# Kernel tuning notes

Measured on AMD Instinct MI355X. Metric: run time of the kernel, lower is better.

The kernel has to match this reference:

```python
import jax, jax.numpy as jnp
import numpy as np
import math

HIDDEN = 512
NUM_HEADS = 8
HEAD_DIM = HIDDEN // NUM_HEADS
NUM_BUCKETS = 32
MAX_DISTANCE = 128


def _relative_position_bucket(rel_pos, bidirectional=True):
    # rel_pos: int32 [S, T]
    num_buckets = NUM_BUCKETS
    ret = 0
    if bidirectional:
        num_buckets //= 2
        ret = (rel_pos > 0).astype(jnp.int32) * num_buckets
        rel_pos = jnp.abs(rel_pos)
    else:
        rel_pos = -jnp.minimum(rel_pos, 0)
    max_exact = num_buckets // 2
    is_small = rel_pos < max_exact
    # guard log(0); result unused where is_small
    safe = jnp.maximum(rel_pos, 1).astype(jnp.float32)
    val_if_large = max_exact + (
        jnp.log(safe / max_exact) / math.log(MAX_DISTANCE / max_exact) * (num_buckets - max_exact)
    ).astype(jnp.int32)
    val_if_large = jnp.minimum(val_if_large, num_buckets - 1)
    return ret + jnp.where(is_small, rel_pos, val_if_large)


def setup_inputs() -> dict:
    key = jax.random.key(0)
    ks = jax.random.split(key, 6)
    B, S = 4, 2048
    std = 1.0 / math.sqrt(HIDDEN)
    inp = {
        "x": jax.random.normal(ks[0], (B, S, HIDDEN), dtype=jnp.float32),
        "Wq": jax.random.normal(ks[1], (HIDDEN, HIDDEN), dtype=jnp.float32) * std,
        "Wk": jax.random.normal(ks[2], (HIDDEN, HIDDEN), dtype=jnp.float32) * std,
        "Wv": jax.random.normal(ks[3], (HIDDEN, HIDDEN), dtype=jnp.float32) * std,
        "Wo": jax.random.normal(ks[4], (HIDDEN, HIDDEN), dtype=jnp.float32) * std,
        "bias_table": jax.random.normal(ks[5], (NUM_BUCKETS, NUM_HEADS), dtype=jnp.float32) * 0.02,
    }
    return inp


def reference(x, Wq, Wk, Wv, Wo, bias_table):
    # x: [B, S, HIDDEN]; weights: [HIDDEN, HIDDEN] (out = x @ W.T semantics folded as x @ W here
    # -- weights are random so orientation is a convention; we use x @ W).
    B, S, _ = x.shape
    T = S  # self-attention, context=None
    scale = HEAD_DIM ** -0.5

    def split_heads(t, L):
        return t.reshape(B, L, NUM_HEADS, HEAD_DIM).transpose(0, 2, 1, 3)  # [B,H,L,D]

    q = split_heads(x @ Wq, S)
    k = split_heads(x @ Wk, T)
    v = split_heads(x @ Wv, T)

    # relative position bias: [1, H, S, T]
    rel = jnp.arange(T, dtype=jnp.int32)[None, :] - jnp.arange(S, dtype=jnp.int32)[:, None]
    buckets = _relative_position_bucket(rel, bidirectional=True)  # [S, T]
    pos_bias = bias_table[buckets]  # [S, T, H]
    pos_bias = pos_bias.transpose(2, 0, 1)[None]  # [1, H, S, T]

    attn = jnp.einsum("bhsd,bhtd->bhst", q, k) * scale + pos_bias
    attn = jax.nn.softmax(attn, axis=-1)  # dropout = identity (eval)
    out = jnp.einsum("bhst,bhtd->bhsd", attn, v)
    out = out.transpose(0, 2, 1, 3).reshape(B, S, HIDDEN)
    return out @ Wo
```

## Files before the change

kernel.cpp:

```cpp
#include <hip/hip_runtime.h>
#include <hip/hip_bf16.h>
#include <math.h>

#define HIDDEN 512
#define NHEADS 8
#define HDIM 64
#define SLEN 2048
#define BATCH 4
#define NROWS (BATCH*SLEN)
#define RTAB (2*SLEN-1)
#define LOG2E 1.44269504088896340736f
#define SCALE_L2E (0.125f * LOG2E)

typedef _Float16 f16;
typedef f16 f16x8 __attribute__((ext_vector_type(8)));
typedef float f32x4 __attribute__((ext_vector_type(4)));
typedef unsigned short u16;
typedef unsigned int u32;
typedef u16 u16x4 __attribute__((ext_vector_type(4)));
typedef u16 u16x8 __attribute__((ext_vector_type(8)));
typedef u32 u32x4 __attribute__((ext_vector_type(4)));

__global__ __launch_bounds__(256) void bias_precompute(
    const float* __restrict__ bias_table, float* __restrict__ biasrel) {
  int i = blockIdx.x * 256 + threadIdx.x;
  if (i >= NHEADS * RTAB) return;
  int h = i / RTAB;
  int idx = i - h * RTAB;
  int rel = idx - (SLEN - 1);
  int ret = rel > 0 ? 16 : 0;
  int a = rel < 0 ? -rel : rel;
  int bidx;
  if (a < 8) {
    bidx = a;
  } else {
    float val = logf((float)a * 0.125f) / logf(16.0f) * 8.0f;
    bidx = 8 + (int)val;
    if (bidx > 15) bidx = 15;
  }
  biasrel[i] = bias_table[(ret + bidx) * NHEADS + h] * LOG2E;
}

__global__ __launch_bounds__(256) void conv_x(
    const float* __restrict__ x, u16* __restrict__ xh) {
  int i = blockIdx.x * 256 + threadIdx.x;
  const float4* p = (const float4*)(x + (size_t)i * 8);
  float4 a = p[0], b = p[1];
  u16x8 o;
  f16 t0 = (f16)a.x; o[0] = *(u16*)&t0;
  f16 t1 = (f16)a.y; o[1] = *(u16*)&t1;
  f16 t2 = (f16)a.z; o[2] = *(u16*)&t2;
  f16 t3 = (f16)a.w; o[3] = *(u16*)&t3;
  f16 t4 = (f16)b.x; o[4] = *(u16*)&t4;
  f16 t5 = (f16)b.y; o[5] = *(u16*)&t5;
  f16 t6 = (f16)b.z; o[6] = *(u16*)&t6;
  f16 t7 = (f16)b.w; o[7] = *(u16*)&t7;
  *(u16x8*)(xh + (size_t)i * 8) = o;
}

__global__ __launch_bounds__(256) void conv_w(
    const float* __restrict__ Wq, const float* __restrict__ Wk,
    const float* __restrict__ Wv, const float* __restrict__ Wo,
    u16* __restrict__ Wt) {
  const float* W = blockIdx.y == 0 ? Wq : blockIdx.y == 1 ? Wk
                 : blockIdx.y == 2 ? Wv : Wo;
  u16* dst = Wt + (size_t)blockIdx.y * HIDDEN * HIDDEN;
  int t = blockIdx.x * 256 + threadIdx.x;
  int k = t >> 6, n0 = (t & 63) << 3;
  const float4* p = (const float4*)(W + (size_t)k * HIDDEN + n0);
  float4 a = p[0], b = p[1];
  float vals[8] = {a.x, a.y, a.z, a.w, b.x, b.y, b.z, b.w};
#pragma unroll
  for (int j = 0; j < 8; ++j) {
    f16 hv = (f16)vals[j];
    dst[(size_t)(n0 + j) * HIDDEN + k] = *(u16*)&hv;
  }
}

__global__ __launch_bounds__(256) void gemm_mfma(
    const u16* __restrict__ A, const u16* __restrict__ Wt0,
    const u16* __restrict__ Wt1, const u16* __restrict__ Wt2,
    void* __restrict__ O, int mode) {
  __shared__ u16 sm[2 * 128 * 72];
  u16 (*As)[72] = (u16(*)[72])sm;
  u16 (*Bs)[72] = (u16(*)[72])(sm + 128 * 72);
  const u16* Wt = blockIdx.z == 0 ? Wt0 : blockIdx.z == 1 ? Wt1 : Wt2;
  const int tid = threadIdx.x;
  const int w = tid >> 6, l = tid & 63;
  const int lr = l & 15, lg = l >> 4;
  const int wr = w >> 1, wc = w & 1;
  const int m0 = blockIdx.x << 7, n0 = blockIdx.y << 7;
  const int vtmode = (mode == 1) && (blockIdx.z == 2);

  f32x4 acc[4][4] = {};

  u16x8 areg[4], breg[4];
#pragma unroll
  for (int e = 0; e < 4; ++e) {
    int c = (e << 8) + tid;
    int row = c >> 3, g = c & 7;
    areg[e] = *(const u16x8*)(A + (size_t)(m0 + row) * HIDDEN + (g << 3));
    breg[e] = *(const u16x8*)(Wt + (size_t)(n0 + row) * HIDDEN + (g << 3));
  }

  for (int k0 = 0; k0 < HIDDEN; k0 += 64) {
    __syncthreads();
#pragma unroll
    for (int e = 0; e < 4; ++e) {
      int c = (e << 8) + tid;
      int row = c >> 3, g = c & 7;
      *(u16x8*)&As[row][g << 3] = areg[e];
      *(u16x8*)&Bs[row][g << 3] = breg[e];
    }
    __syncthreads();
    if (k0 + 64 < HIDDEN) {
#pragma unroll
      for (int e = 0; e < 4; ++e) {
        int c = (e << 8) + tid;
        int row = c >> 3, g = c & 7;
        areg[e] = *(const u16x8*)(A + (size_t)(m0 + row) * HIDDEN + k0 + 64 + (g << 3));
        breg[e] = *(const u16x8*)(Wt + (size_t)(n0 + row) * HIDDEN + k0 + 64 + (g << 3));
      }
    }
#pragma unroll
    for (int kk = 0; kk < 64; kk += 32) {
      f16x8 af[4], bf[4];
#pragma unroll
      for (int mt = 0; mt < 4; ++mt)
        af[mt] = *(const f16x8*)&As[(wr << 6) + (mt << 4) + lr][kk + (lg << 3)];
#pragma unroll
      for (int nt = 0; nt < 4; ++nt)
        bf[nt] = *(const f16x8*)&Bs[(wc << 6) + (nt << 4) + lr][kk + (lg << 3)];
      if (!vtmode) {
#pragma unroll
        for (int mt = 0; mt < 4; ++mt)
#pragma unroll
          for (int nt = 0; nt < 4; ++nt)
            acc[mt][nt] = __builtin_amdgcn_mfma_f32_16x16x32_f16(
                af[mt], bf[nt], acc[mt][nt], 0, 0, 0);
      } else {
#pragma unroll
        for (int i = 0; i < 4; ++i)
#pragma unroll
          for (int j = 0; j < 4; ++j)
            acc[i][j] = __builtin_amdgcn_mfma_f32_16x16x32_f16(
                bf[i], af[j], acc[i][j], 0, 0, 0);
      }
    }
  }

  if (mode == 0) {
    float* Of = (float*)O;
#pragma unroll
    for (int mt = 0; mt < 4; ++mt)
#pragma unroll
      for (int nt = 0; nt < 4; ++nt)
#pragma unroll
        for (int r = 0; r < 4; ++r) {
          int m = m0 + (wr << 6) + (mt << 4) + (lg << 2) + r;
          int n = n0 + (wc << 6) + (nt << 4) + lr;
          Of[(size_t)m * HIDDEN + n] = acc[mt][nt][r];
        }
  } else if (!vtmode) {
    u16* O16 = (u16*)O + (size_t)blockIdx.z * NROWS * HIDDEN;
    const float osc = (blockIdx.z == 0) ? SCALE_L2E : 1.0f;
#pragma unroll
    for (int mt = 0; mt < 4; ++mt)
#pragma unroll
      for (int nt = 0; nt < 4; ++nt)
#pragma unroll
        for (int r = 0; r < 4; ++r) {
          int m = m0 + (wr << 6) + (mt << 4) + (lg << 2) + r;
          int n = n0 + (wc << 6) + (nt << 4) + lr;
          int b = m >> 11, s = m & (SLEN - 1);
          int h = n >> 6, d = n & 63;
          f16 hv = (f16)(acc[mt][nt][r] * osc);
          O16[(((size_t)b * NHEADS + h) * SLEN + s) * HDIM + d] = *(u16*)&hv;
        }
  } else {
    __syncthreads();
    u16* tt = sm;
#pragma unroll
    for (int i = 0; i < 4; ++i)
#pragma unroll
      for (int j = 0; j < 4; ++j)
#pragma unroll
        for (int r = 0; r < 4; ++r) {
          int nl = (wc << 6) + (i << 4) + (lg << 2) + r;
          int ml = (wr << 6) + (j << 4) + lr;
          f16 hv = (f16)acc[i][j][r];
          tt[nl * 136 + ml] = *(u16*)&hv;
        }
    __syncthreads();
    u16* O16 = (u16*)O + (size_t)2 * NROWS * HIDDEN;
    int nl = tid >> 1, half = tid & 1;
    int n = n0 + nl;
    int h = n >> 6, d = n & 63;
    int b = m0 >> 11, s_base = m0 & (SLEN - 1);
    u16* orow = O16 + (((size_t)b * NHEADS + h) * HDIM + d) * SLEN + s_base;
    const u16* trow = tt + nl * 136;
#pragma unroll
    for (int c = 0; c < 8; ++c) {
      int v_off = (half << 6) + (c << 3);
      int c0 = (v_off & ~31) | (((v_off >> 3) & 3) << 2);
      u16x4 lo = *(const u16x4*)(trow + c0);
      u16x4 hi = *(const u16x4*)(trow + c0 + 16);
      u16x8 st;
#pragma unroll
      for (int j = 0; j < 4; ++j) { st[j] = lo[j]; st[j + 4] = hi[j]; }
      *(u16x8*)(orow + v_off) = st;
    }
  }
}

__global__ __launch_bounds__(256) void flash_attn_mfma(
    const u16* __restrict__ qg, const u16* __restrict__ kg,
    const u16* __restrict__ vtg, const float* __restrict__ biasrel,
    u16* __restrict__ attn_out) {
  __shared__ u16 Ks[2][64][72];
  __shared__ u16 Vt[2][64][72];

  const int tid = threadIdx.x;
  const int w = tid >> 6, l = tid & 63;
  const int lr = l & 15, lg = l >> 4;

  int bid = blockIdx.x;
  int xcd = bid & 7, idx = bid >> 3;
  int bh = (xcd << 2) + (idx >> 4);
  int bx = idx & 15;
  int h = bh & 7, b = bh >> 3;
  int q0 = bx << 7;

  const u16* qp = qg + (size_t)bh * (SLEN * HDIM);
  const u16* kp = kg + (size_t)bh * (SLEN * HDIM);
  const u16* vp = vtg + (size_t)bh * (HDIM * SLEN);

  const float bias_pos = biasrel[h * RTAB + 2 * (SLEN - 1)];
  const float bias_neg = biasrel[h * RTAB];

  f16x8 aq[2][2];
#pragma unroll
  for (int sub = 0; sub < 2; ++sub) {
    const u16* qrow = qp + (size_t)(q0 + (w << 5) + (sub << 4) + lr) * HDIM + (lg << 3);
    aq[sub][0] = *(const f16x8*)(qrow);
    aq[sub][1] = *(const f16x8*)(qrow + 32);
  }

  const float* bb = biasrel + h * RTAB + (SLEN - 1) + (lg << 2) - lr - q0 - (w << 5);

  f32x4 acc[2][4] = {};
  float l_run[2] = {0.f, 0.f};

  u16x8 kreg[2], vreg[2];
#pragma unroll
  for (int e = 0; e < 2; ++e) {
    int c = tid + (e << 8);
    int row = c >> 3, c8 = (c & 7) << 3;
    kreg[e] = *(const u16x8*)(kp + (size_t)row * HDIM + c8);
    vreg[e] = *(const u16x8*)(vp + (size_t)row * SLEN + c8);
  }
#pragma unroll
  for (int e = 0; e < 2; ++e) {
    int c = tid + (e << 8);
    int row = c >> 3, c8 = (c & 7) << 3;
    *(u16x8*)&Ks[0][row][c8] = kreg[e];
    *(u16x8*)&Vt[0][row][c8] = vreg[e];
  }
#pragma unroll
  for (int e = 0; e < 2; ++e) {
    int c = tid + (e << 8);
    int row = c >> 3, c8 = (c & 7) << 3;
    kreg[e] = *(const u16x8*)(kp + (size_t)(64 + row) * HDIM + c8);
    vreg[e] = *(const u16x8*)(vp + (size_t)row * SLEN + 64 + c8);
  }
  __syncthreads();

  int cur = 0;
  for (int t0 = 0; t0 < SLEN; t0 += 64) {
    if (t0 + 64 < SLEN) {
#pragma unroll
      for (int e = 0; e < 2; ++e) {
        int c = tid + (e << 8);
        int row = c >> 3, c8 = (c & 7) << 3;
        *(u16x8*)&Ks[cur ^ 1][row][c8] = kreg[e];
        *(u16x8*)&Vt[cur ^ 1][row][c8] = vreg[e];
      }
      if (t0 + 128 < SLEN) {
#pragma unroll
        for (int e = 0; e < 2; ++e) {
          int c = tid + (e << 8);
          int row = c >> 3, c8 = (c & 7) << 3;
          kreg[e] = *(const u16x8*)(kp + (size_t)(t0 + 128 + row) * HDIM + c8);
          vreg[e] = *(const u16x8*)(vp + (size_t)row * SLEN + t0 + 128 + c8);
        }
      }
    }

    int dtq = t0 - q0;
    f32x4 sc[2][4];
    if (dtq >= 256 || dtq <= -192) {
      float c = (dtq > 0) ? bias_pos : bias_neg;
      f32x4 cv = {c, c, c, c};
#pragma unroll
      for (int sub = 0; sub < 2; ++sub)
#pragma unroll
        for (int ct = 0; ct < 4; ++ct) sc[sub][ct] = cv;
    } else {
#pragma unroll
      for (int sub = 0; sub < 2; ++sub)
#pragma unroll
        for (int ct = 0; ct < 4; ++ct)
#pragma unroll
          for (int r = 0; r < 4; ++r)
            sc[sub][ct][r] = bb[t0 + (ct << 4) + r - (sub << 4)];
    }

    f16x8 kf[4][2];
#pragma unroll
    for (int ct = 0; ct < 4; ++ct) {
      kf[ct][0] = *(const f16x8*)&Ks[cur][(ct << 4) + lr][lg << 3];
      kf[ct][1] = *(const f16x8*)&Ks[cur][(ct << 4) + lr][32 + (lg << 3)];
    }

    __builtin_amdgcn_s_setprio(1);
#pragma unroll
    for (int sub = 0; sub < 2; ++sub)
#pragma unroll
      for (int ct = 0; ct < 4; ++ct) {
        sc[sub][ct] = __builtin_amdgcn_mfma_f32_16x16x32_f16(
            kf[ct][0], aq[sub][0], sc[sub][ct], 0, 0, 0);
        sc[sub][ct] = __builtin_amdgcn_mfma_f32_16x16x32_f16(
            kf[ct][1], aq[sub][1], sc[sub][ct], 0, 0, 0);
      }
    __builtin_amdgcn_s_setprio(0);

#pragma unroll
    for (int sub = 0; sub < 2; ++sub) {
      float rs = 0.f;
#pragma unroll
      for (int ct = 0; ct < 4; ++ct)
#pragma unroll
        for (int r = 0; r < 4; ++r) {
          float pe = __builtin_amdgcn_exp2f(sc[sub][ct][r]);
          sc[sub][ct][r] = pe;
          rs += pe;
        }
      l_run[sub] += rs;
    }

    f16x8 vf[2][4];
#pragma unroll
    for (int kb = 0; kb < 2; ++kb)
#pragma unroll
      for (int dt = 0; dt < 4; ++dt)
        vf[kb][dt] = *(const f16x8*)&Vt[cur][(dt << 4) + lr][(kb << 5) + (lg << 3)];

    __builtin_amdgcn_s_setprio(1);
#pragma unroll
    for (int sub = 0; sub < 2; ++sub)
#pragma unroll
      for (int kb = 0; kb < 2; ++kb) {
        u32 a0 = __builtin_bit_cast(u32,
            __builtin_amdgcn_cvt_pkrtz(sc[sub][2 * kb][0], sc[sub][2 * kb][1]));
        u32 a1 = __builtin_bit_cast(u32,
            __builtin_amdgcn_cvt_pkrtz(sc[sub][2 * kb][2], sc[sub][2 * kb][3]));
        u32 a2 = __builtin_bit_cast(u32,
            __builtin_amdgcn_cvt_pkrtz(sc[sub][2 * kb + 1][0], sc[sub][2 * kb + 1][1]));
        u32 a3 = __builtin_bit_cast(u32,
            __builtin_amdgcn_cvt_pkrtz(sc[sub][2 * kb + 1][2], sc[sub][2 * kb + 1][3]));
        u32x4 pk = {a0, a1, a2, a3};
        f16x8 pa = __builtin_bit_cast(f16x8, pk);
#pragma unroll
        for (int dt = 0; dt < 4; ++dt)
          acc[sub][dt] = __builtin_amdgcn_mfma_f32_16x16x32_f16(
              pa, vf[kb][dt], acc[sub][dt], 0, 0, 0);
      }
    __builtin_amdgcn_s_setprio(0);

    __syncthreads();
    cur ^= 1;
  }

#pragma unroll
  for (int sub = 0; sub < 2; ++sub) {
    float lt = l_run[sub];
    lt += __shfl_xor(lt, 16, 64);
    lt += __shfl_xor(lt, 32, 64);
    float linv[4];
#pragma unroll
    for (int r = 0; r < 4; ++r) linv[r] = 1.f / __shfl(lt, (lg << 2) + r, 16);
    u16* op = attn_out +
              ((size_t)(b * SLEN) + q0 + (w << 5) + (sub << 4)) * HIDDEN + (h << 6);
#pragma unroll
    for (int r = 0; r < 4; ++r)
#pragma unroll
      for (int dt = 0; dt < 4; ++dt) {
        f16 hv = (f16)(acc[sub][dt][r] * linv[r]);
        op[(size_t)((lg << 2) + r) * HIDDEN + (dt << 4) + lr] = *(u16*)&hv;
      }
  }
}

extern "C" void kernel_launch(void* const* d_in, const int* in_sizes, int n_in,
                              void* d_out, int out_size, void* d_ws, size_t ws_size,
                              hipStream_t stream) {
  const float* x          = (const float*)d_in[0];
  const float* Wq         = (const float*)d_in[1];
  const float* Wk         = (const float*)d_in[2];
  const float* Wv         = (const float*)d_in[3];
  const float* Wo         = (const float*)d_in[4];
  const float* bias_table = (const float*)d_in[5];
  float* out = (float*)d_out;

  u16* xh   = (u16*)d_ws;
  u16* wt   = xh + (size_t)NROWS * HIDDEN;
  u16* qkv  = wt + (size_t)4 * HIDDEN * HIDDEN;
  u16* attno_h = qkv + (size_t)3 * NROWS * HIDDEN;
  float* biasrel = (float*)(attno_h + (size_t)NROWS * HIDDEN);

  u16* qb = qkv;
  u16* kb = qkv + (size_t)NROWS * HIDDEN;
  u16* vb = qkv + (size_t)2 * NROWS * HIDDEN;

  bias_precompute<<<(NHEADS * RTAB + 255) / 256, 256, 0, stream>>>(bias_table, biasrel);
  conv_x<<<NROWS * HIDDEN / 8 / 256, 256, 0, stream>>>(x, xh);
  conv_w<<<dim3(HIDDEN * HIDDEN / 8 / 256, 4), 256, 0, stream>>>(Wq, Wk, Wv, Wo, wt);

  u16* wtq = wt;
  u16* wtk = wt + (size_t)HIDDEN * HIDDEN;
  u16* wtv = wt + (size_t)2 * HIDDEN * HIDDEN;
  u16* wto = wt + (size_t)3 * HIDDEN * HIDDEN;

  gemm_mfma<<<dim3(NROWS / 128, HIDDEN / 128, 3), 256, 0, stream>>>(
      xh, wtq, wtk, wtv, qkv, 1);

  flash_attn_mfma<<<SLEN / 128 * BATCH * NHEADS, 256, 0, stream>>>(
      qb, kb, vb, biasrel, attno_h);

  gemm_mfma<<<dim3(NROWS / 128, HIDDEN / 128, 1), 256, 0, stream>>>(
      attno_h, wto, wto, wto, out, 0);
}
```

Baseline: 105.6 us.

## Use direct global-to-LDS loads with XOR-swizzled layout in QKV projection GEMM

The QKV projection GEMM (mode 1) now loads A and W tiles straight into LDS with global_load_lds, skipping the register staging step. To keep LDS reads free of bank conflicts without padding, the fp16 conversion kernels write x and the transposed weights in an XOR-swizzled chunk order, and the MFMA fragment reads undo that swizzle. The mode-0 output GEMM keeps register staging but un-swizzles W on load. The mode-1 path drops the software prefetch overlap and uses single buffering, so load latency may be less hidden.

```diff
diff --git a/kernel.cpp b/kernel.cpp
--- a/kernel.cpp
+++ b/kernel.cpp
@@ -20,6 +20,13 @@
 typedef u16 u16x4 __attribute__((ext_vector_type(4)));
 typedef u16 u16x8 __attribute__((ext_vector_type(8)));
 typedef u32 u32x4 __attribute__((ext_vector_type(4)));
+
+typedef const __attribute__((address_space(1))) void gvoid;
+typedef __attribute__((address_space(3))) void lvoid;
+
+static __device__ __forceinline__ void gload16(const void* g, void* l) {
+  __builtin_amdgcn_global_load_lds((gvoid*)g, (lvoid*)l, 16, 0, 0);
+}
 
 __global__ __launch_bounds__(256) void bias_precompute(
     const float* __restrict__ bias_table, float* __restrict__ biasrel) {
@@ -55,7 +62,9 @@
   f16 t5 = (f16)b.y; o[5] = *(u16*)&t5;
   f16 t6 = (f16)b.z; o[6] = *(u16*)&t6;
   f16 t7 = (f16)b.w; o[7] = *(u16*)&t7;
-  *(u16x8*)(xh + (size_t)i * 8) = o;
+  int m = i >> 6;
+  int ch = (i & 63) ^ (m & 7);
+  *(u16x8*)(xh + (size_t)m * HIDDEN + (ch << 3)) = o;
 }
 
 __global__ __launch_bounds__(256) void conv_w(
@@ -72,8 +81,10 @@
   float vals[8] = {a.x, a.y, a.z, a.w, b.x, b.y, b.z, b.w};
 #pragma unroll
   for (int j = 0; j < 8; ++j) {
+    int n = n0 + j;
+    int chsw = (k >> 3) ^ (n & 7);
     f16 hv = (f16)vals[j];
-    dst[(size_t)(n0 + j) * HIDDEN + k] = *(u16*)&hv;
+    dst[(size_t)n * HIDDEN + (chsw << 3) + (k & 7)] = *(u16*)&hv;
   }
 }
 
@@ -82,8 +93,6 @@
     const u16* __restrict__ Wt1, const u16* __restrict__ Wt2,
     void* __restrict__ O, int mode) {
   __shared__ u16 sm[2 * 128 * 72];
-  u16 (*As)[72] = (u16(*)[72])sm;
-  u16 (*Bs)[72] = (u16(*)[72])(sm + 128 * 72);
   const u16* Wt = blockIdx.z == 0 ? Wt0 : blockIdx.z == 1 ? Wt1 : Wt2;
   const int tid = threadIdx.x;
   const int w = tid >> 6, l = tid & 63;
@@ -94,59 +103,101 @@
 
   f32x4 acc[4][4] = {};
 
-  u16x8 areg[4], breg[4];
-#pragma unroll
-  for (int e = 0; e < 4; ++e) {
-    int c = (e << 8) + tid;
-    int row = c >> 3, g = c & 7;
-    areg[e] = *(const u16x8*)(A + (size_t)(m0 + row) * HIDDEN + (g << 3));
-    breg[e] = *(const u16x8*)(Wt + (size_t)(n0 + row) * HIDDEN + (g << 3));
-  }
-
-  for (int k0 = 0; k0 < HIDDEN; k0 += 64) {
-    __syncthreads();
+  if (mode == 1) {
+    u16* AsL = sm;
+    u16* BsL = sm + 128 * 64;
+    const int gr = (l >> 3), gc = (l & 7) << 3;
+    for (int k0 = 0; k0 < HIDDEN; k0 += 64) {
+#pragma unroll
+      for (int i = 0; i < 4; ++i) {
+        int r0 = (w << 5) + (i << 3);
+        gload16(A + (size_t)(m0 + r0 + gr) * HIDDEN + k0 + gc, AsL + (r0 << 6));
+        gload16(Wt + (size_t)(n0 + r0 + gr) * HIDDEN + k0 + gc, BsL + (r0 << 6));
+      }
+      __syncthreads();
+#pragma unroll
+      for (int kk = 0; kk < 64; kk += 32) {
+        f16x8 af[4], bf[4];
+#pragma unroll
+        for (int mt = 0; mt < 4; ++mt) {
+          int row = (wr << 6) + (mt << 4) + lr;
+          af[mt] = *(const f16x8*)(AsL + (row << 6) +
+                                   ((((kk >> 3) + lg) ^ (lr & 7)) << 3));
+        }
+#pragma unroll
+        for (int nt = 0; nt < 4; ++nt) {
+          int row = (wc << 6) + (nt << 4) + lr;
+          bf[nt] = *(const f16x8*)(BsL + (row << 6) +
+                                   ((((kk >> 3) + lg) ^ (lr & 7)) << 3));
+        }
+        if (!vtmode) {
+#pragma unroll
+          for (int mt = 0; mt < 4; ++mt)
+#pragma unroll
+            for (int nt = 0; nt < 4; ++nt)
+              acc[mt][nt] = __builtin_amdgcn_mfma_f32_16x16x32_f16(
+                  af[mt], bf[nt], acc[mt][nt], 0, 0, 0);
+        } else {
+#pragma unroll
+          for (int i = 0; i < 4; ++i)
+#pragma unroll
+            for (int j = 0; j < 4; ++j)
+              acc[i][j] = __builtin_amdgcn_mfma_f32_16x16x32_f16(
+                  bf[i], af[j], acc[i][j], 0, 0, 0);
+        }
+      }
+      __syncthreads();
+    }
+  } else {
+    u16 (*As)[72] = (u16(*)[72])sm;
+    u16 (*Bs)[72] = (u16(*)[72])(sm + 128 * 72);
+    u16x8 areg[4], breg[4];
 #pragma unroll
     for (int e = 0; e < 4; ++e) {
       int c = (e << 8) + tid;
       int row = c >> 3, g = c & 7;
-      *(u16x8*)&As[row][g << 3] = areg[e];
-      *(u16x8*)&Bs[row][g << 3] = breg[e];
-    }
-    __syncthreads();
-    if (k0 + 64 < HIDDEN) {
+      areg[e] = *(const u16x8*)(A + (size_t)(m0 + row) * HIDDEN + (g << 3));
+      breg[e] = *(const u16x8*)(Wt + (size_t)(n0 + row) * HIDDEN +
+                                ((g ^ (row & 7)) << 3));
+    }
+    for (int k0 = 0; k0 < HIDDEN; k0 += 64) {
+      __syncthreads();
 #pragma unroll
       for (int e = 0; e < 4; ++e) {
         int c = (e << 8) + tid;
         int row = c >> 3, g = c & 7;
-        areg[e] = *(const u16x8*)(A + (size_t)(m0 + row) * HIDDEN + k0 + 64 + (g << 3));
-        breg[e] = *(const u16x8*)(Wt + (size_t)(n0 + row) * HIDDEN + k0 + 64 + (g << 3));
-      }
-    }
-#pragma unroll
-    for (int kk = 0; kk < 64; kk += 32) {
-      f16x8 af[4], bf[4];
-#pragma unroll
-      for (int mt = 0; mt < 4; ++mt)
-        af[mt] = *(const f16x8*)&As[(wr << 6) + (mt << 4) + lr][kk + (lg << 3)];
-#pragma unroll
-      for (int nt = 0; nt < 4; ++nt)
-        bf[nt] = *(const f16x8*)&Bs[(wc << 6) + (nt << 4) + lr][kk + (lg << 3)];
-      if (!vtmode) {
+        *(u16x8*)&As[row][g << 3] = areg[e];
+        *(u16x8*)&Bs[row][g << 3] = breg[e];
+      }
+      __syncthreads();
+      if (k0 + 64 < HIDDEN) {
+#pragma unroll
+        for (int e = 0; e < 4; ++e) {
+          int c = (e << 8) + tid;
+          int row = c >> 3, g = c & 7;
+          areg[e] = *(const u16x8*)(A + (size_t)(m0 + row) * HIDDEN + k0 + 64 + (g << 3));
+          breg[e] = *(const u16x8*)(Wt + (size_t)(n0 + row) * HIDDEN + k0 + 64 +
+                                    ((g ^ (row & 7)) << 3));
+        }
+      }
+#pragma unroll
+      for (int kk = 0; kk < 64; kk += 32) {
+        f16x8 af[4], bf[4];
+#pragma unroll
+        for (int mt = 0; mt < 4; ++mt)
+          af[mt] = *(const f16x8*)&As[(wr << 6) + (mt << 4) + lr][kk + (lg << 3)];
+#pragma unroll
+        for (int nt = 0; nt < 4; ++nt)
+          bf[nt] = *(const f16x8*)&Bs[(wc << 6) + (nt << 4) + lr][kk + (lg << 3)];
 #pragma unroll
         for (int mt = 0; mt < 4; ++mt)
 #pragma unroll
           for (int nt = 0; nt < 4; ++nt)
             acc[mt][nt] = __builtin_amdgcn_mfma_f32_16x16x32_f16(
                 af[mt], bf[nt], acc[mt][nt], 0, 0, 0);
-      } else {
-#pragma unroll
-        for (int i = 0; i < 4; ++i)
-#pragma unroll
-          for (int j = 0; j < 4; ++j)
-            acc[i][j] = __builtin_amdgcn_mfma_f32_16x16x32_f16(
-                bf[i], af[j], acc[i][j], 0, 0, 0);
-      }
-    }
+      }
+    }
+    __syncthreads();
   }
 
   if (mode == 0) {
@@ -178,7 +229,6 @@
           O16[(((size_t)b * NHEADS + h) * SLEN + s) * HDIM + d] = *(u16*)&hv;
         }
   } else {
-    __syncthreads();
     u16* tt = sm;
 #pragma unroll
     for (int i = 0; i < 4; ++i)
```

Result: no change. 107.6 us (+1.9%).

## Split key tiles across wave pairs and reduce partial attention outputs in LDS

Applied to the files above, without the earlier changes.

Waves are regrouped into two query groups of 64 rows each, and the two waves in a group take alternate 64-key tiles. Each wave therefore reuses every loaded K/V fragment across four query sub-tiles instead of two, cutting LDS fragment reads per MFMA. At the end the partial accumulators and row sums from the odd-key waves go through shared memory and are added into the even-key waves before normalization. This adds a final LDS reduction and barrier and raises register pressure (acc[4][4]). Half the waves also sit idle on each tile iteration, which may reduce overlap.

```diff
diff --git a/kernel.cpp b/kernel.cpp
--- a/kernel.cpp
+++ b/kernel.cpp
@@ -217,12 +217,14 @@
     const u16* __restrict__ qg, const u16* __restrict__ kg,
     const u16* __restrict__ vtg, const float* __restrict__ biasrel,
     u16* __restrict__ attn_out) {
-  __shared__ u16 Ks[2][64][72];
-  __shared__ u16 Vt[2][64][72];
+  __shared__ __align__(16) u16 sbuf[4 * 64 * 72];
+  u16 (*Ks)[64][72] = (u16(*)[64][72])sbuf;
+  u16 (*Vt)[64][72] = (u16(*)[64][72])(sbuf + 2 * 64 * 72);
 
   const int tid = threadIdx.x;
   const int w = tid >> 6, l = tid & 63;
   const int lr = l & 15, lg = l >> 4;
+  const int wq = w >> 1, wk = w & 1;
 
   int bid = blockIdx.x;
   int xcd = bid & 7, idx = bid >> 3;
@@ -238,18 +240,18 @@
   const float bias_pos = biasrel[h * RTAB + 2 * (SLEN - 1)];
   const float bias_neg = biasrel[h * RTAB];
 
-  f16x8 aq[2][2];
-#pragma unroll
-  for (int sub = 0; sub < 2; ++sub) {
-    const u16* qrow = qp + (size_t)(q0 + (w << 5) + (sub << 4) + lr) * HDIM + (lg << 3);
+  f16x8 aq[4][2];
+#pragma unroll
+  for (int sub = 0; sub < 4; ++sub) {
+    const u16* qrow = qp + (size_t)(q0 + (wq << 6) + (sub << 4) + lr) * HDIM + (lg << 3);
     aq[sub][0] = *(const f16x8*)(qrow);
     aq[sub][1] = *(const f16x8*)(qrow + 32);
   }
 
-  const float* bb = biasrel + h * RTAB + (SLEN - 1) + (lg << 2) - lr - q0 - (w << 5);
-
-  f32x4 acc[2][4] = {};
-  float l_run[2] = {0.f, 0.f};
+  const float* bb = biasrel + h * RTAB + (SLEN - 1) + (lg << 2) - lr - q0 - (wq << 6);
+
+  f32x4 acc[4][4] = {};
+  float l_run[4] = {0.f, 0.f, 0.f, 0.f};
 
   u16x8 kreg[2], vreg[2];
 #pragma unroll
@@ -296,108 +298,134 @@
       }
     }
 
-    int dtq = t0 - q0;
-    f32x4 sc[2][4];
-    if (dtq >= 256 || dtq <= -192) {
-      float c = (dtq > 0) ? bias_pos : bias_neg;
-      f32x4 cv = {c, c, c, c};
-#pragma unroll
-      for (int sub = 0; sub < 2; ++sub)
-#pragma unroll
-        for (int ct = 0; ct < 4; ++ct) sc[sub][ct] = cv;
-    } else {
-#pragma unroll
-      for (int sub = 0; sub < 2; ++sub)
+    if (((t0 >> 6) & 1) == wk) {
+      int dtq = t0 - q0;
+      const int far = (dtq >= 256 || dtq <= -192);
+      const float cfar = (dtq > 0) ? bias_pos : bias_neg;
+
+      f16x8 kf[4][2];
+#pragma unroll
+      for (int ct = 0; ct < 4; ++ct) {
+        kf[ct][0] = *(const f16x8*)&Ks[cur][(ct << 4) + lr][lg << 3];
+        kf[ct][1] = *(const f16x8*)&Ks[cur][(ct << 4) + lr][32 + (lg << 3)];
+      }
+      f16x8 vf[2][4];
+#pragma unroll
+      for (int kb = 0; kb < 2; ++kb)
+#pragma unroll
+        for (int dt = 0; dt < 4; ++dt)
+          vf[kb][dt] = *(const f16x8*)&Vt[cur][(dt << 4) + lr][(kb << 5) + (lg << 3)];
+
+#pragma unroll
+      for (int sub = 0; sub < 4; ++sub) {
+        f32x4 sc[4];
+        if (far) {
+          f32x4 cv = {cfar, cfar, cfar, cfar};
+#pragma unroll
+          for (int ct = 0; ct < 4; ++ct) sc[ct] = cv;
+        } else {
+#pragma unroll
+          for (int ct = 0; ct < 4; ++ct)
+#pragma unroll
+            for (int r = 0; r < 4; ++r)
+              sc[ct][r] = bb[t0 + (ct << 4) + r - (sub << 4)];
+        }
+
+        __builtin_amdgcn_s_setprio(1);
+#pragma unroll
+        for (int ct = 0; ct < 4; ++ct) {
+          sc[ct] = __builtin_amdgcn_mfma_f32_16x16x32_f16(
+              kf[ct][0], aq[sub][0], sc[ct], 0, 0, 0);
+          sc[ct] = __builtin_amdgcn_mfma_f32_16x16x32_f16(
+              kf[ct][1], aq[sub][1], sc[ct], 0, 0, 0);
+        }
+        __builtin_amdgcn_s_setprio(0);
+
+        float rs = 0.f;
 #pragma unroll
         for (int ct = 0; ct < 4; ++ct)
 #pragma unroll
-          for (int r = 0; r < 4; ++r)
-            sc[sub][ct][r] = bb[t0 + (ct << 4) + r - (sub << 4)];
-    }
-
-    f16x8 kf[4][2];
-#pragma unroll
-    for (int ct = 0; ct < 4; ++ct) {
-      kf[ct][0] = *(const f16x8*)&Ks[cur][(ct << 4) + lr][lg << 3];
-      kf[ct][1] = *(const f16x8*)&Ks[cur][(ct << 4) + lr][32 + (lg << 3)];
-    }
-
-    __builtin_amdgcn_s_setprio(1);
-#pragma unroll
-    for (int sub = 0; sub < 2; ++sub)
-#pragma unroll
-      for (int ct = 0; ct < 4; ++ct) {
-        sc[sub][ct] = __builtin_amdgcn_mfma_f32_16x16x32_f16(
-            kf[ct][0], aq[sub][0], sc[sub][ct], 0, 0, 0);
-        sc[sub][ct] = __builtin_amdgcn_mfma_f32_16x16x32_f16(
-            kf[ct][1], aq[sub][1], sc[sub][ct], 0, 0, 0);
-      }
-    __builtin_amdgcn_s_setprio(0);
-
-#pragma unroll
-    for (int sub = 0; sub < 2; ++sub) {
-      float rs = 0.f;
-#pragma unroll
-      for (int ct = 0; ct < 4; ++ct)
-#pragma unroll
-        for (int r = 0; r < 4; ++r) {
-          float pe = __builtin_amdgcn_exp2f(sc[sub][ct][r]);
-          sc[sub][ct][r] = pe;
-          rs += pe;
-        }
-      l_run[sub] += rs;
-    }
-
-    f16x8 vf[2][4];
-#pragma unroll
-    for (int kb = 0; kb < 2; ++kb)
-#pragma unroll
-      for (int dt = 0; dt < 4; ++dt)
-        vf[kb][dt] = *(const f16x8*)&Vt[cur][(dt << 4) + lr][(kb << 5) + (lg << 3)];
-
-    __builtin_amdgcn_s_setprio(1);
-#pragma unroll
-    for (int sub = 0; sub < 2; ++sub)
-#pragma unroll
-      for (int kb = 0; kb < 2; ++kb) {
-        u32 a0 = __builtin_bit_cast(u32,
-            __builtin_amdgcn_cvt_pkrtz(sc[sub][2 * kb][0], sc[sub][2 * kb][1]));
-        u32 a1 = __builtin_bit_cast(u32,
-            __builtin_amdgcn_cvt_pkrtz(sc[sub][2 * kb][2], sc[sub][2 * kb][3]));
-        u32 a2 = __builtin_bit_cast(u32,
-            __builtin_amdgcn_cvt_pkrtz(sc[sub][2 * kb + 1][0], sc[sub][2 * kb + 1][1]));
-        u32 a3 = __builtin_bit_cast(u32,
-            __builtin_amdgcn_cvt_pkrtz(sc[sub][2 * kb + 1][2], sc[sub][2 * kb + 1][3]));
-        u32x4 pk = {a0, a1, a2, a3};
-        f16x8 pa = __builtin_bit_cast(f16x8, pk);
-#pragma unroll
-        for (int dt = 0; dt < 4; ++dt)
-          acc[sub][dt] = __builtin_amdgcn_mfma_f32_16x16x32_f16(
-              pa, vf[kb][dt], acc[sub][dt], 0, 0, 0);
-      }
-    __builtin_amdgcn_s_setprio(0);
+          for (int r = 0; r < 4; ++r) {
+            float pe = __builtin_amdgcn_exp2f(sc[ct][r]);
+            sc[ct][r] = pe;
+            rs += pe;
+          }
+        l_run[sub] += rs;
+
+        __builtin_amdgcn_s_setprio(1);
+#pragma unroll
+        for (int kb = 0; kb < 2; ++kb) {
+          u32 a0 = __builtin_bit_cast(u32,
+              __builtin_amdgcn_cvt_pkrtz(sc[2 * kb][0], sc[2 * kb][1]));
+          u32 a1 = __builtin_bit_cast(u32,
+              __builtin_amdgcn_cvt_pkrtz(sc[2 * kb][2], sc[2 * kb][3]));
+          u32 a2 = __builtin_bit_cast(u32,
+              __builtin_amdgcn_cvt_pkrtz(sc[2 * kb + 1][0], sc[2 * kb + 1][1]));
+          u32 a3 = __builtin_bit_cast(u32,
+              __builtin_amdgcn_cvt_pkrtz(sc[2 * kb + 1][2], sc[2 * kb + 1][3]));
+          u32x4 pk = {a0, a1, a2, a3};
+          f16x8 pa = __builtin_bit_cast(f16x8, pk);
+#pragma unroll
+          for (int dt = 0; dt < 4; ++dt)
+            acc[sub][dt] = __builtin_amdgcn_mfma_f32_16x16x32_f16(
+                pa, vf[kb][dt], acc[sub][dt], 0, 0, 0);
+        }
+        __builtin_amdgcn_s_setprio(0);
+      }
+    }
 
     __syncthreads();
     cur ^= 1;
   }
 
-#pragma unroll
-  for (int sub = 0; sub < 2; ++sub) {
-    float lt = l_run[sub];
-    lt += __shfl_xor(lt, 16, 64);
-    lt += __shfl_xor(lt, 32, 64);
-    float linv[4];
-#pragma unroll
-    for (int r = 0; r < 4; ++r) linv[r] = 1.f / __shfl(lt, (lg << 2) + r, 16);
-    u16* op = attn_out +
-              ((size_t)(b * SLEN) + q0 + (w << 5) + (sub << 4)) * HIDDEN + (h << 6);
-#pragma unroll
-    for (int r = 0; r < 4; ++r)
-#pragma unroll
-      for (int dt = 0; dt < 4; ++dt) {
-        f16 hv = (f16)(acc[sub][dt][r] * linv[r]);
-        op[(size_t)((lg << 2) + r) * HIDDEN + (dt << 4) + lr] = *(u16*)&hv;
-      }
+  float lt[4];
+#pragma unroll
+  for (int sub = 0; sub < 4; ++sub) {
+    float t = l_run[sub];
+    t += __shfl_xor(t, 16, 64);
+    t += __shfl_xor(t, 32, 64);
+    lt[sub] = t;
+  }
+
+  float* red = (float*)sbuf;
+  float* redl = (float*)sbuf + 8192;
+
+  if (wk == 1) {
+#pragma unroll
+    for (int sub = 0; sub < 4; ++sub)
+#pragma unroll
+      for (int dt = 0; dt < 4; ++dt)
+        *(f32x4*)&red[(((((wq << 2) + sub) << 2) + dt) << 8) + (l << 2)] = acc[sub][dt];
+    if (lg == 0)
+#pragma unroll
+      for (int sub = 0; sub < 4; ++sub)
+        redl[(((wq << 2) + sub) << 4) + lr] = lt[sub];
+  }
+  __syncthreads();
+  if (wk == 0) {
+#pragma unroll
+    for (int sub = 0; sub < 4; ++sub) {
+#pragma unroll
+      for (int dt = 0; dt < 4; ++dt)
+        acc[sub][dt] += *(const f32x4*)
+            &red[(((((wq << 2) + sub) << 2) + dt) << 8) + (l << 2)];
+      lt[sub] += redl[(((wq << 2) + sub) << 4) + lr];
+    }
+#pragma unroll
+    for (int sub = 0; sub < 4; ++sub) {
+      float linv[4];
+#pragma unroll
+      for (int r = 0; r < 4; ++r) linv[r] = 1.f / __shfl(lt[sub], (lg << 2) + r, 16);
+      u16* op = attn_out +
+                ((size_t)(b * SLEN) + q0 + (wq << 6) + (sub << 4)) * HIDDEN + (h << 6);
+#pragma unroll
+      for (int r = 0; r < 4; ++r)
+#pragma unroll
+        for (int dt = 0; dt < 4; ++dt) {
+          f16 hv = (f16)(acc[sub][dt][r] * linv[r]);
+          op[(size_t)((lg << 2) + r) * HIDDEN + (dt << 4) + lr] = *(u16*)&hv;
+        }
+    }
   }
 }
 
```

After: 182.8 us. +73.0%, slower.
